# Kernel tuning notes

Hardware: AMD Instinct MI355X
Metric: run time of the kernel (lower is better)

The kernel has to match this reference:

```python
import jax, jax.numpy as jnp
import numpy as np

# ViT-Tiny + Performer attention (eval mode: dropout/droppath are no-ops)
B = 64
IMG, PATCH, GRID = 224, 16, 14
NPATCH, NTOK = 196, 197
EMBED, HEADS, HEAD_DIM = 192, 3, 64
DEPTH, FEAT, MLP, NCLS = 12, 256, 768, 1000
EXIT_IDXS = [4, 8, 12]
LN_EPS = 1e-5


def _ln(x, w, b):
    mu = x.mean(-1, keepdims=True)
    var = ((x - mu) ** 2).mean(-1, keepdims=True)
    return (x - mu) / jnp.sqrt(var + LN_EPS) * w + b


def setup_inputs() -> dict:
    key = jax.random.key(0)
    ks = jax.random.split(key, 16)
    n = lambda k, shape, s=0.02: jax.random.normal(k, shape, jnp.float32) * s
    inp = {}
    inp["x"] = jax.random.normal(ks[0], (B, 3, IMG, IMG), jnp.float32)
    inp["patch_w"] = n(ks[1], (EMBED, 3, PATCH, PATCH))
    inp["patch_b"] = jnp.zeros((EMBED,), jnp.float32)
    inp["pe_norm_w"] = jnp.ones((EMBED,), jnp.float32)
    inp["pe_norm_b"] = jnp.zeros((EMBED,), jnp.float32)
    inp["cls_token"] = n(ks[2], (1, 1, EMBED))
    inp["pos_embed"] = n(ks[3], (1, NTOK, EMBED))
    inp["norm1_w"] = jnp.ones((DEPTH, EMBED), jnp.float32)
    inp["norm1_b"] = jnp.zeros((DEPTH, EMBED), jnp.float32)
    inp["qkv_w"] = n(ks[4], (DEPTH, EMBED, 3 * EMBED))
    inp["qkv_b"] = jnp.zeros((DEPTH, 3 * EMBED), jnp.float32)
    # Gaussian random projection matrix (stands in for the orthogonal RF matrix)
    inp["proj_mat"] = jax.random.normal(ks[5], (DEPTH, FEAT, HEAD_DIM), jnp.float32)
    inp["attn_proj_w"] = n(ks[6], (DEPTH, EMBED, EMBED))
    inp["attn_proj_b"] = jnp.zeros((DEPTH, EMBED), jnp.float32)
    inp["norm2_w"] = jnp.ones((DEPTH, EMBED), jnp.float32)
    inp["norm2_b"] = jnp.zeros((DEPTH, EMBED), jnp.float32)
    inp["fc1_w"] = n(ks[7], (DEPTH, EMBED, MLP))
    inp["fc1_b"] = jnp.zeros((DEPTH, MLP), jnp.float32)
    inp["fc2_w"] = n(ks[8], (DEPTH, MLP, EMBED))
    inp["fc2_b"] = jnp.zeros((DEPTH, EMBED), jnp.float32)
    inp["exit_w"] = n(ks[9], (len(EXIT_IDXS), EMBED, NCLS))
    inp["exit_b"] = jnp.zeros((len(EXIT_IDXS), NCLS), jnp.float32)
    inp["final_norm_w"] = jnp.ones((EMBED,), jnp.float32)
    inp["final_norm_b"] = jnp.zeros((EMBED,), jnp.float32)
    inp["head_w"] = n(ks[10], (EMBED, NCLS))
    inp["head_b"] = jnp.zeros((NCLS,), jnp.float32)
    return inp


def _performer_attn(x, qw, qb, pm, pw, pb):
    Bn, N, C = x.shape
    qkv = (x @ qw + qb).reshape(Bn, N, 3, HEADS, HEAD_DIM).transpose(2, 0, 3, 1, 4)
    q, k, v = qkv[0], qkv[1], qkv[2]  # [B,H,N,d]

    def fmap(t):
        proj = jnp.einsum('bhnd,fd->bhnf', t, pm)  # random-feature projection
        norm_t = jnp.sum(t * t, axis=-1, keepdims=True) / 2.0
        return jnp.exp(proj - norm_t) * (HEAD_DIM ** -0.25)

    pq = fmap(q)  # [B,H,N,F]
    pk = fmap(k)
    k_cumsum = pk.sum(axis=2)  # [B,H,F]
    D_inv = 1.0 / jnp.einsum('bhnf,bhf->bhn', pq, k_cumsum)
    attn = jnp.einsum('bhnf,bhmf->bhnm', pq, pk)  # as in original (materializes NxN)
    out = jnp.einsum('bhnm,bhmd->bhnd', attn, v)
    out = out * D_inv[..., None]
    out = out.transpose(0, 2, 1, 3).reshape(Bn, N, C)
    return out @ pw + pb


def reference(x, patch_w, patch_b, pe_norm_w, pe_norm_b, cls_token, pos_embed,
              norm1_w, norm1_b, qkv_w, qkv_b, proj_mat, attn_proj_w, attn_proj_b,
              norm2_w, norm2_b, fc1_w, fc1_b, fc2_w, fc2_b,
              exit_w, exit_b, final_norm_w, final_norm_b, head_w, head_b):
    Bn = x.shape[0]
    # PatchEmbed: non-overlapping 16x16 conv == reshape + matmul (c,ph,pw order)
    p = x.reshape(Bn, 3, GRID, PATCH, GRID, PATCH).transpose(0, 2, 4, 1, 3, 5)
    p = p.reshape(Bn, NPATCH, 3 * PATCH * PATCH)
    tok = p @ patch_w.reshape(EMBED, -1).T + patch_b
    tok = _ln(tok, pe_norm_w, pe_norm_b)
    cls = jnp.broadcast_to(cls_token, (Bn, 1, EMBED))
    h = jnp.concatenate([cls, tok], axis=1) + pos_embed  # [B,197,192]

    exits = []
    for i in range(DEPTH):
        a = _performer_attn(_ln(h, norm1_w[i], norm1_b[i]), qkv_w[i], qkv_b[i],
                            proj_mat[i], attn_proj_w[i], attn_proj_b[i])
        h = h + a
        m = _ln(h, norm2_w[i], norm2_b[i])
        m = jax.nn.gelu(m @ fc1_w[i] + fc1_b[i], approximate=False) @ fc2_w[i] + fc2_b[i]
        h = h + m
        if (i + 1) in EXIT_IDXS:
            e = EXIT_IDXS.index(i + 1)
            z = h.mean(axis=1)  # AdaptiveAvgPool1d(1) over tokens
            exits.append(z @ exit_w[e] + exit_b[e])

    hf = _ln(h, final_norm_w, final_norm_b)
    logits = hf[:, 0] @ head_w + head_b  # cls-token head
    return (logits, exits[0], exits[1], exits[2])
```

## Files before the change

### kernel.cpp

```cpp
#include <hip/hip_runtime.h>
#include <math.h>

typedef unsigned short u16;
typedef unsigned int u32;
typedef __attribute__((ext_vector_type(8))) short short8;
typedef __attribute__((ext_vector_type(4))) float floatx4;

#define BB 64
#define NTOK 197
#define NPATCH 196
#define EMB 192
#define NH 3
#define HD 64
#define FEAT 256
#define MLPD 768
#define NCLS 1000
#define MTOT (BB*NTOK)
#define MPAT (BB*NPATCH)
#define BHT (BB*NH)

__device__ __forceinline__ u16 f2bf(float x) {
    u32 u = __builtin_bit_cast(u32, x);
    u32 r = u + 0x7FFFu + ((u >> 16) & 1u);
    return (u16)(r >> 16);
}
__device__ __forceinline__ float bf2f(u16 u) {
    return __builtin_bit_cast(float, (u32)u << 16);
}
__device__ __forceinline__ float sqr8bf(uint4 v) {
    float s = 0.f;
    float t;
    t = bf2f((u16)(v.x & 0xffff)); s += t*t;  t = bf2f((u16)(v.x >> 16)); s += t*t;
    t = bf2f((u16)(v.y & 0xffff)); s += t*t;  t = bf2f((u16)(v.y >> 16)); s += t*t;
    t = bf2f((u16)(v.z & 0xffff)); s += t*t;  t = bf2f((u16)(v.z >> 16)); s += t*t;
    t = bf2f((u16)(v.w & 0xffff)); s += t*t;  t = bf2f((u16)(v.w >> 16)); s += t*t;
    return s;
}

__global__ void cvt_bf16(const float* __restrict__ in, u16* __restrict__ out, int n)
{
    const int i = blockIdx.x * 256 + threadIdx.x;
    if (i < n) out[i] = f2bf(in[i]);
}

__global__ void tr_bf16_t(const float* __restrict__ in, u16* __restrict__ out,
                          int R, int C)
{
    __shared__ u16 t[32][33];
    const int l = blockIdx.z;
    const int c0 = blockIdx.x * 32, r0 = blockIdx.y * 32;
    const int tx = threadIdx.x & 31, ty = threadIdx.x >> 5;
    const float* ip = in + ((size_t)l * R + r0) * C + c0;
#pragma unroll
    for (int j = 0; j < 4; ++j)
        t[ty + j*8][tx] = f2bf(ip[(size_t)(ty + j*8) * C + tx]);
    __syncthreads();
    u16* op = out + ((size_t)l * C + c0) * R + r0;
#pragma unroll
    for (int j = 0; j < 4; ++j)
        op[(size_t)(ty + j*8) * R + tx] = t[tx][ty + j*8];
}

__global__ void tr_bf16_g(const float* __restrict__ in, u16* __restrict__ out,
                          int R, int C)
{
    __shared__ u16 t[32][33];
    const int l = blockIdx.z;
    const int c0 = blockIdx.x * 32, r0 = blockIdx.y * 32;
    const int tx = threadIdx.x & 31, ty = threadIdx.x >> 5;
    const float* ip = in + (size_t)l * R * C;
#pragma unroll
    for (int j = 0; j < 4; ++j) {
        const int r = r0 + ty + j*8, c = c0 + tx;
        t[ty + j*8][tx] = (r < R && c < C) ? f2bf(ip[(size_t)r * C + c]) : (u16)0;
    }
    __syncthreads();
    u16* op = out + (size_t)l * C * R;
#pragma unroll
    for (int j = 0; j < 4; ++j) {
        const int c = c0 + ty + j*8, r = r0 + tx;
        if (c < C && r < R)
            op[(size_t)c * R + r] = t[tx][ty + j*8];
    }
}

__global__ __launch_bounds__(256) void gemm_bf16(
    const u16* __restrict__ A, const u16* __restrict__ Bt,
    const float* __restrict__ bias,
    float* __restrict__ Cf, u16* __restrict__ Cb,
    int M, int N, int K, int mode, int ntx)
{
    __shared__ u16 As[128][72];
    __shared__ u16 Bs[64][72];
    const int tid = threadIdx.x;
    const int lane = tid & 63, wave = tid >> 6;
    const int l16 = lane & 15, quad = lane >> 4;
    const int nwg = gridDim.x;
    const int q = nwg >> 3, r = nwg & 7;
    const int xcd = blockIdx.x & 7, jj = blockIdx.x >> 3;
    const int wg = (xcd < r ? xcd * (q + 1) : r * (q + 1) + (xcd - r) * q) + jj;
    const int m0 = (wg / ntx) * 128, n0 = (wg % ntx) * 64;
    const int arow = tid >> 1, aof = (tid & 1) * 32;
    const int brow = tid >> 2, bof = (tid & 3) * 16;

    floatx4 acc[2][4];
#pragma unroll
    for (int i = 0; i < 2; ++i)
#pragma unroll
        for (int j = 0; j < 4; ++j) acc[i][j] = (floatx4){0.f,0.f,0.f,0.f};

    const int gmA = m0 + arow;
    const bool aok = (gmA < M);
    const u16* ap = A + (size_t)gmA * K + aof;
    const u16* bp = Bt + (size_t)(n0 + brow) * K + bof;

    for (int k0 = 0; k0 < K; k0 += 64) {
        uint4 a0 = {0,0,0,0}, a1 = {0,0,0,0}, a2 = {0,0,0,0}, a3 = {0,0,0,0};
        if (aok) {
            a0 = *(const uint4*)(ap + k0);
            a1 = *(const uint4*)(ap + k0 + 8);
            a2 = *(const uint4*)(ap + k0 + 16);
            a3 = *(const uint4*)(ap + k0 + 24);
        }
        const uint4 b0 = *(const uint4*)(bp + k0);
        const uint4 b1 = *(const uint4*)(bp + k0 + 8);
        if (k0) __syncthreads();
        *(uint4*)&As[arow][aof]      = a0;
        *(uint4*)&As[arow][aof + 8]  = a1;
        *(uint4*)&As[arow][aof + 16] = a2;
        *(uint4*)&As[arow][aof + 24] = a3;
        *(uint4*)&Bs[brow][bof]      = b0;
        *(uint4*)&Bs[brow][bof + 8]  = b1;
        __syncthreads();
#pragma unroll
        for (int ks = 0; ks < 2; ++ks) {
            short8 af[2], bf[4];
#pragma unroll
            for (int rf = 0; rf < 2; ++rf)
                af[rf] = *(const short8*)&As[wave*32 + rf*16 + l16][ks*32 + quad*8];
#pragma unroll
            for (int cf = 0; cf < 4; ++cf)
                bf[cf] = *(const short8*)&Bs[cf*16 + l16][ks*32 + quad*8];
#pragma unroll
            for (int rf = 0; rf < 2; ++rf)
#pragma unroll
                for (int cf = 0; cf < 4; ++cf)
                    acc[rf][cf] = __builtin_amdgcn_mfma_f32_16x16x32_bf16(af[rf], bf[cf], acc[rf][cf], 0, 0, 0);
        }
    }

    if (mode == 0) {
        const int rbase = m0 + wave * 32 + quad * 4;
        const int cbase = n0 + l16;
#pragma unroll
        for (int rf = 0; rf < 2; ++rf) {
#pragma unroll
            for (int reg = 0; reg < 4; ++reg) {
                const int gm = rbase + rf * 16 + reg;
                if (gm >= M) continue;
#pragma unroll
                for (int cf = 0; cf < 4; ++cf) {
                    const int gn = cbase + cf * 16;
                    Cf[(size_t)gm * N + gn] = acc[rf][cf][reg] + bias[gn];
                }
            }
        }
        return;
    }

    __syncthreads();
#pragma unroll
    for (int rf = 0; rf < 2; ++rf) {
#pragma unroll
        for (int cf = 0; cf < 4; ++cf) {
            const int lc = cf * 16 + l16;
            const float bia = bias[n0 + lc];
#pragma unroll
            for (int reg = 0; reg < 4; ++reg) {
                const int lr = wave * 32 + rf * 16 + quad * 4 + reg;
                const float v = acc[rf][cf][reg] + bia;
                const int phys = (((lc >> 3) ^ (lr & 7)) << 3) | (lc & 7);
                As[lr][phys] = f2bf(v);
            }
        }
    }
    __syncthreads();
#pragma unroll
    for (int it = 0; it < 4; ++it) {
        const int idx = it * 256 + tid;
        const int row = idx >> 3, c8 = idx & 7;
        const int pc8 = c8 ^ (row & 7);
        const uint4 val = *(const uint4*)&As[row][pc8 * 8];
        const int gm = m0 + row;
        if (gm < M)
            *(uint4*)&Cb[(size_t)gm * N + n0 + c8 * 8] = val;
    }
}

__global__ __launch_bounds__(256) void gemm_ln(
    const u16* __restrict__ A, const u16* __restrict__ Bt,
    const float* __restrict__ bias,
    const float* __restrict__ lnw, const float* __restrict__ lnb,
    float* __restrict__ H, u16* __restrict__ outb, int K)
{
    __shared__ u16 As[32][72];
    __shared__ u16 Bs[192][72];
    __shared__ float red_s[2][32][2];
    const int tid = threadIdx.x;
    const int lane = tid & 63, wave = tid >> 6;
    const int wr = wave & 1;
    const int wc = wave >> 1;
    const int l16 = lane & 15, quad = lane >> 4;
    const int m0 = blockIdx.x * 32;
    const int srowA = tid >> 3, skofA = (tid & 7) * 8;
    const int srow = tid >> 2, skof = (tid & 3) * 16;

    floatx4 acc[6];
#pragma unroll
    for (int j = 0; j < 6; ++j) acc[j] = (floatx4){0.f,0.f,0.f,0.f};

    const u16* ap = A + (size_t)(m0 + srowA) * K + skofA;
    const u16* bp = Bt + (size_t)srow * K + skof;
    const size_t bstep = (size_t)64 * K;

    for (int k0 = 0; k0 < K; k0 += 64) {
        const uint4 a0 = *(const uint4*)(ap + k0);
        const uint4 b0 = *(const uint4*)(bp + k0);
        const uint4 b1 = *(const uint4*)(bp + k0 + 8);
        const uint4 b2 = *(const uint4*)(bp + bstep + k0);
        const uint4 b3 = *(const uint4*)(bp + bstep + k0 + 8);
        const uint4 b4 = *(const uint4*)(bp + 2*bstep + k0);
        const uint4 b5 = *(const uint4*)(bp + 2*bstep + k0 + 8);
        if (k0) __syncthreads();
        *(uint4*)&As[srowA][skofA]         = a0;
        *(uint4*)&Bs[srow][skof]           = b0;
        *(uint4*)&Bs[srow][skof + 8]       = b1;
        *(uint4*)&Bs[srow + 64][skof]      = b2;
        *(uint4*)&Bs[srow + 64][skof + 8]  = b3;
        *(uint4*)&Bs[srow + 128][skof]     = b4;
        *(uint4*)&Bs[srow + 128][skof + 8] = b5;
        __syncthreads();
#pragma unroll
        for (int ks = 0; ks < 2; ++ks) {
            const short8 af = *(const short8*)&As[wr*16 + l16][ks*32 + quad*8];
            short8 bf[6];
#pragma unroll
            for (int cf = 0; cf < 6; ++cf)
                bf[cf] = *(const short8*)&Bs[wc*96 + cf*16 + l16][ks*32 + quad*8];
#pragma unroll
            for (int cf = 0; cf < 6; ++cf)
                acc[cf] = __builtin_amdgcn_mfma_f32_16x16x32_bf16(af, bf[cf], acc[cf], 0, 0, 0);
        }
    }

    float s_[4], q_[4];
#pragma unroll
    for (int reg = 0; reg < 4; ++reg) { s_[reg] = 0.f; q_[reg] = 0.f; }

#pragma unroll
    for (int cf = 0; cf < 6; ++cf) {
        const int gn = wc * 96 + cf * 16 + l16;
        const float bia = bias[gn];
#pragma unroll
        for (int reg = 0; reg < 4; ++reg) {
            const int gm = m0 + wr * 16 + quad * 4 + reg;
            float v = acc[cf][reg] + bia + H[(size_t)gm * EMB + gn];
            H[(size_t)gm * EMB + gn] = v;
            acc[cf][reg] = v;
            s_[reg] += v;
            q_[reg] += v * v;
        }
    }

    if (lnw) {
#pragma unroll
        for (int reg = 0; reg < 4; ++reg) {
            float s = s_[reg], q = q_[reg];
            s += __shfl_xor(s, 1); q += __shfl_xor(q, 1);
            s += __shfl_xor(s, 2); q += __shfl_xor(q, 2);
            s += __shfl_xor(s, 4); q += __shfl_xor(q, 4);
            s += __shfl_xor(s, 8); q += __shfl_xor(q, 8);
            if (l16 == 0) {
                const int rl = wr * 16 + quad * 4 + reg;
                red_s[wc][rl][0] = s;
                red_s[wc][rl][1] = q;
            }
        }
        __syncthreads();
#pragma unroll
        for (int reg = 0; reg < 4; ++reg) {
            const int rl = wr * 16 + quad * 4 + reg;
            const float ts = red_s[0][rl][0] + red_s[1][rl][0];
            const float tq = red_s[0][rl][1] + red_s[1][rl][1];
            const float mu = ts * (1.f / 192.f);
            const float var = tq * (1.f / 192.f) - mu * mu;
            const float rstd = rsqrtf(fmaxf(var, 0.f) + 1e-5f);
            const int gm = m0 + rl;
#pragma unroll
            for (int cf = 0; cf < 6; ++cf) {
                const int gn = wc * 96 + cf * 16 + l16;
                const float y = (acc[cf][reg] - mu) * rstd * lnw[gn] + lnb[gn];
                outb[(size_t)gm * EMB + gn] = f2bf(y);
            }
        }
    }
}

__global__ __launch_bounds__(256) void mlp_ln(
    const u16* __restrict__ A, const u16* __restrict__ W1t,
    const float* __restrict__ b1,
    const u16* __restrict__ W2t, const float* __restrict__ b2,
    const float* __restrict__ lnw, const float* __restrict__ lnb,
    float* __restrict__ H, u16* __restrict__ outb)
{
    __shared__ u16 As[32][200];
    __shared__ u16 W1s[64][200];
    __shared__ u16 W2s[192][72];
    __shared__ u16 Ms[32][72];
    __shared__ float red_s[4][32][2];
    const int tid = threadIdx.x;
    const int lane = tid & 63, wave = tid >> 6;
    const int l16 = lane & 15, quad = lane >> 4;
    const int m0 = blockIdx.x * 32;

    {
        const int row = tid >> 3, cb = (tid & 7) * 24;
        const u16* ap = A + (size_t)(m0 + row) * EMB + cb;
#pragma unroll
        for (int j = 0; j < 3; ++j)
            *(uint4*)&As[row][cb + j * 8] = *(const uint4*)(ap + j * 8);
    }
    __syncthreads();
    short8 af[2][6];
#pragma unroll
    for (int rf = 0; rf < 2; ++rf)
#pragma unroll
        for (int ks = 0; ks < 6; ++ks)
            af[rf][ks] = *(const short8*)&As[rf*16 + l16][ks*32 + quad*8];

    floatx4 acc[2][3];
#pragma unroll
    for (int i = 0; i < 2; ++i)
#pragma unroll
        for (int j = 0; j < 3; ++j) acc[i][j] = (floatx4){0.f,0.f,0.f,0.f};

    for (int c = 0; c < 12; ++c) {
        if (c) __syncthreads();
        {
            const int row = tid >> 2, cb = (tid & 3) * 48;
            const u16* wp = W1t + (size_t)(c * 64 + row) * EMB + cb;
#pragma unroll
            for (int j = 0; j < 6; ++j)
                *(uint4*)&W1s[row][cb + j * 8] = *(const uint4*)(wp + j * 8);
        }
#pragma unroll
        for (int j = 0; j < 6; ++j) {
            const int idx = j * 256 + tid;
            const int e = idx >> 3, o = (idx & 7) * 8;
            *(uint4*)&W2s[e][o] = *(const uint4*)(W2t + (size_t)e * MLPD + c * 64 + o);
        }
        __syncthreads();

        floatx4 mf[2] = {(floatx4){0.f,0.f,0.f,0.f}, (floatx4){0.f,0.f,0.f,0.f}};
#pragma unroll
        for (int ks = 0; ks < 6; ++ks) {
            const short8 w1f = *(const short8*)&W1s[wave*16 + l16][ks*32 + quad*8];
            mf[0] = __builtin_amdgcn_mfma_f32_16x16x32_bf16(af[0][ks], w1f, mf[0], 0, 0, 0);
            mf[1] = __builtin_amdgcn_mfma_f32_16x16x32_bf16(af[1][ks], w1f, mf[1], 0, 0, 0);
        }
        const float bia = b1[c * 64 + wave * 16 + l16];
#pragma unroll
        for (int rf = 0; rf < 2; ++rf)
#pragma unroll
            for (int reg = 0; reg < 4; ++reg) {
                float v = mf[rf][reg] + bia;
                v = 0.5f * v * (1.f + erff(v * 0.70710678118654752f));
                Ms[rf*16 + quad*4 + reg][wave*16 + l16] = f2bf(v);
            }
        __syncthreads();

#pragma unroll
        for (int ks2 = 0; ks2 < 2; ++ks2) {
            short8 a2[2], w2f[3];
#pragma unroll
            for (int rf = 0; rf < 2; ++rf)
                a2[rf] = *(const short8*)&Ms[rf*16 + l16][ks2*32 + quad*8];
#pragma unroll
            for (int cf = 0; cf < 3; ++cf)
                w2f[cf] = *(const short8*)&W2s[wave*48 + cf*16 + l16][ks2*32 + quad*8];
#pragma unroll
            for (int rf = 0; rf < 2; ++rf)
#pragma unroll
                for (int cf = 0; cf < 3; ++cf)
                    acc[rf][cf] = __builtin_amdgcn_mfma_f32_16x16x32_bf16(a2[rf], w2f[cf], acc[rf][cf], 0, 0, 0);
        }
    }

    float s_[2][4], q_[2][4];
#pragma unroll
    for (int rf = 0; rf < 2; ++rf)
#pragma unroll
        for (int reg = 0; reg < 4; ++reg) { s_[rf][reg] = 0.f; q_[rf][reg] = 0.f; }

#pragma unroll
    for (int rf = 0; rf < 2; ++rf) {
#pragma unroll
        for (int cf = 0; cf < 3; ++cf) {
            const int gn = wave * 48 + cf * 16 + l16;
            const float bia = b2[gn];
#pragma unroll
            for (int reg = 0; reg < 4; ++reg) {
                const int gm = m0 + rf * 16 + quad * 4 + reg;
                float v = acc[rf][cf][reg] + bia + H[(size_t)gm * EMB + gn];
                H[(size_t)gm * EMB + gn] = v;
                acc[rf][cf][reg] = v;
                s_[rf][reg] += v;
                q_[rf][reg] += v * v;
            }
        }
    }

    if (lnw) {
#pragma unroll
        for (int rf = 0; rf < 2; ++rf)
#pragma unroll
            for (int reg = 0; reg < 4; ++reg) {
                float s = s_[rf][reg], q = q_[rf][reg];
                s += __shfl_xor(s, 1); q += __shfl_xor(q, 1);
                s += __shfl_xor(s, 2); q += __shfl_xor(q, 2);
                s += __shfl_xor(s, 4); q += __shfl_xor(q, 4);
                s += __shfl_xor(s, 8); q += __shfl_xor(q, 8);
                if (l16 == 0) {
                    const int rl = rf * 16 + quad * 4 + reg;
                    red_s[wave][rl][0] = s;
                    red_s[wave][rl][1] = q;
                }
            }
        __syncthreads();
#pragma unroll
        for (int rf = 0; rf < 2; ++rf) {
#pragma unroll
            for (int reg = 0; reg < 4; ++reg) {
                const int rl = rf * 16 + quad * 4 + reg;
                const float ts = red_s[0][rl][0] + red_s[1][rl][0]
                               + red_s[2][rl][0] + red_s[3][rl][0];
                const float tq = red_s[0][rl][1] + red_s[1][rl][1]
                               + red_s[2][rl][1] + red_s[3][rl][1];
                const float mu = ts * (1.f / 192.f);
                const float var = tq * (1.f / 192.f) - mu * mu;
                const float rstd = rsqrtf(fmaxf(var, 0.f) + 1e-5f);
                const int gm = m0 + rl;
#pragma unroll
                for (int cf = 0; cf < 3; ++cf) {
                    const int gn = wave * 48 + cf * 16 + l16;
                    const float y = (acc[rf][cf][reg] - mu) * rstd * lnw[gn] + lnb[gn];
                    outb[(size_t)gm * EMB + gn] = f2bf(y);
                }
            }
        }
    }
}

__global__ __launch_bounds__(256) void attn_pkv(
    const u16* __restrict__ qkv, const u16* __restrict__ pmb,
    u16* __restrict__ kvT, float* __restrict__ ksum)
{
    __shared__ u16 pm_s[64][72];
    __shared__ u16 kt_s[64][72];
    __shared__ u16 vT_s[64][72];
    __shared__ u16 pkT_s[64][72];
    __shared__ float nrm_s[64];
    __shared__ float ksum_s[64];

    const int tid = threadIdx.x;
    const int lane = tid & 63, wave = tid >> 6;
    const int l16 = lane & 15, quad = lane >> 4;
    const int fq = blockIdx.x, bh = blockIdx.y, b = bh / NH, h = bh % NH;
    const int fwave = wave * 16;
    const int srow = tid >> 2, skof = (tid & 3) * 16;
    const float scale = 0.35355339059327373f;

#pragma unroll
    for (int j = 0; j < 2; ++j) {
        const int flat = j * 256 + tid;
        const int row = flat >> 3, o = (flat & 7) * 8;
        *(uint4*)&pm_s[row][o] = *(const uint4*)(pmb + (size_t)(fq * 64 + row) * 64 + o);
    }
    if (tid < 64) ksum_s[tid] = 0.f;

    floatx4 kv[4];
#pragma unroll
    for (int i = 0; i < 4; ++i) kv[i] = (floatx4){0.f,0.f,0.f,0.f};

    uint4 k0v = {0,0,0,0}, k1v = {0,0,0,0}, v0v = {0,0,0,0}, v1v = {0,0,0,0};
    {
        const u16* kp = qkv + ((size_t)(b * NTOK + srow)) * 576 + 192 + h * 64 + skof;
        k0v = *(const uint4*)kp; k1v = *(const uint4*)(kp + 8);
        v0v = *(const uint4*)(kp + 192); v1v = *(const uint4*)(kp + 200);
    }

    for (int t = 0; t < 4; ++t) {
        const int ncur = t * 64 + srow;
        if (t) __syncthreads();
        *(uint4*)&kt_s[srow][skof]     = k0v;
        *(uint4*)&kt_s[srow][skof + 8] = k1v;
        {
            u16 vv[16];
            vv[0]=(u16)(v0v.x&0xffff);  vv[1]=(u16)(v0v.x>>16);
            vv[2]=(u16)(v0v.y&0xffff);  vv[3]=(u16)(v0v.y>>16);
            vv[4]=(u16)(v0v.z&0xffff);  vv[5]=(u16)(v0v.z>>16);
            vv[6]=(u16)(v0v.w&0xffff);  vv[7]=(u16)(v0v.w>>16);
            vv[8]=(u16)(v1v.x&0xffff);  vv[9]=(u16)(v1v.x>>16);
            vv[10]=(u16)(v1v.y&0xffff); vv[11]=(u16)(v1v.y>>16);
            vv[12]=(u16)(v1v.z&0xffff); vv[13]=(u16)(v1v.z>>16);
            vv[14]=(u16)(v1v.w&0xffff); vv[15]=(u16)(v1v.w>>16);
#pragma unroll
            for (int j = 0; j < 16; ++j) vT_s[skof + j][srow] = vv[j];
        }
        float sq = sqr8bf(k0v) + sqr8bf(k1v);
        sq += __shfl_xor(sq, 1);
        sq += __shfl_xor(sq, 2);
        if ((tid & 3) == 0) nrm_s[srow] = (ncur < NTOK) ? 0.5f * sq : 1e30f;
        __syncthreads();

        if (t < 3) {
            const int n = (t + 1) * 64 + srow;
            k0v = (uint4){0,0,0,0}; k1v = (uint4){0,0,0,0};
            v0v = (uint4){0,0,0,0}; v1v = (uint4){0,0,0,0};
            if (n < NTOK) {
                const u16* kp = qkv + ((size_t)(b * NTOK + n)) * 576 + 192 + h * 64 + skof;
                k0v = *(const uint4*)kp; k1v = *(const uint4*)(kp + 8);
                v0v = *(const uint4*)(kp + 192); v1v = *(const uint4*)(kp + 200);
            }
        }

        floatx4 pa[4];
#pragma unroll
        for (int i = 0; i < 4; ++i) pa[i] = (floatx4){0.f,0.f,0.f,0.f};
#pragma unroll
        for (int ks = 0; ks < 2; ++ks) {
            const short8 bpm = *(const short8*)&pm_s[fwave + l16][ks*32 + quad*8];
#pragma unroll
            for (int rf = 0; rf < 4; ++rf) {
                const short8 a = *(const short8*)&kt_s[rf*16 + l16][ks*32 + quad*8];
                pa[rf] = __builtin_amdgcn_mfma_f32_16x16x32_bf16(a, bpm, pa[rf], 0, 0, 0);
            }
        }

        float ksp = 0.f;
        const int floc = fwave + l16;
#pragma unroll
        for (int rf = 0; rf < 4; ++rf) {
            const int nl = rf * 16 + quad * 4;
            const u16 b0 = f2bf(__expf(pa[rf][0] - nrm_s[nl + 0]) * scale);
            const u16 b1 = f2bf(__expf(pa[rf][1] - nrm_s[nl + 1]) * scale);
            const u16 b2 = f2bf(__expf(pa[rf][2] - nrm_s[nl + 2]) * scale);
            const u16 b3 = f2bf(__expf(pa[rf][3] - nrm_s[nl + 3]) * scale);
            ksp += bf2f(b0) + bf2f(b1) + bf2f(b2) + bf2f(b3);
            *(u32*)&pkT_s[floc][nl]     = (u32)b0 | ((u32)b1 << 16);
            *(u32*)&pkT_s[floc][nl + 2] = (u32)b2 | ((u32)b3 << 16);
        }
        {
            float v = ksp;
            v += __shfl_xor(v, 16);
            v += __shfl_xor(v, 32);
            if (quad == 0) ksum_s[floc] += v;
        }

#pragma unroll
        for (int ks = 0; ks < 2; ++ks) {
            const short8 bpk = *(const short8*)&pkT_s[fwave + l16][ks*32 + quad*8];
#pragma unroll
            for (int rf = 0; rf < 4; ++rf) {
                const short8 a = *(const short8*)&vT_s[rf*16 + l16][ks*32 + quad*8];
                kv[rf] = __builtin_amdgcn_mfma_f32_16x16x32_bf16(a, bpk, kv[rf], 0, 0, 0);
            }
        }
    }

    __syncthreads();
    if (tid < 64) ksum[(size_t)bh * 256 + fq * 64 + tid] = ksum_s[tid];
    const int fg = fq * 64 + fwave + l16;
#pragma unroll
    for (int rf = 0; rf < 4; ++rf) {
#pragma unroll
        for (int reg = 0; reg < 4; ++reg) {
            const int d = rf * 16 + quad * 4 + reg;
            kvT[((size_t)bh * 64 + d) * 256 + fg] = f2bf(kv[rf][reg]);
        }
    }
}

__global__ __launch_bounds__(256) void attn_out(
    const u16* __restrict__ qkv, const u16* __restrict__ pmb,
    const u16* __restrict__ kvT, const float* __restrict__ ksum,
    u16* __restrict__ attn_o)
{
    __shared__ u16 pm_s[256][72];
    __shared__ u16 q_s[64][72];
    __shared__ u16 pq_s[64][264];
    __shared__ u16 kv_s[64][264];
    __shared__ float nrm_s[64];
    __shared__ float den_s[4][64];

    const int tid = threadIdx.x;
    const int lane = tid & 63, wave = tid >> 6;
    const int l16 = lane & 15, quad = lane >> 4;
    const int bh = blockIdx.y, b = bh / NH, h = bh % NH;
    const int n0 = blockIdx.x * 64;
    const int fbase = wave * 64;
    const int srow = tid >> 2, skof = (tid & 3) * 16;
    const float scale = 0.35355339059327373f;

#pragma unroll
    for (int j = 0; j < 8; ++j) {
        const int flat = j * 256 + tid;
        const int f = flat >> 3, o = (flat & 7) * 8;
        *(uint4*)&pm_s[f][o] = *(const uint4*)(pmb + f * 64 + o);
    }
#pragma unroll
    for (int j = 0; j < 8; ++j) {
        const int flat = j * 256 + tid;
        const int d = flat >> 5, o = (flat & 31) * 8;
        *(uint4*)&kv_s[d][o] = *(const uint4*)(kvT + ((size_t)bh * 64 + d) * 256 + o);
    }
    {
        const int n = n0 + srow;
        uint4 q0 = {0,0,0,0}, q1 = {0,0,0,0};
        if (n < NTOK) {
            const u16* qp = qkv + ((size_t)(b * NTOK + n)) * 576 + h * 64 + skof;
            q0 = *(const uint4*)qp; q1 = *(const uint4*)(qp + 8);
        }
        *(uint4*)&q_s[srow][skof]     = q0;
        *(uint4*)&q_s[srow][skof + 8] = q1;
        float sq = sqr8bf(q0) + sqr8bf(q1);
        sq += __shfl_xor(sq, 1);
        sq += __shfl_xor(sq, 2);
        if ((tid & 3) == 0) nrm_s[srow] = (n < NTOK) ? 0.5f * sq : 1e30f;
    }
    float ksr[4];
#pragma unroll
    for (int cf = 0; cf < 4; ++cf)
        ksr[cf] = ksum[(size_t)bh * 256 + fbase + cf * 16 + l16];
    __syncthreads();

    floatx4 pa[4][4];
#pragma unroll
    for (int i = 0; i < 4; ++i)
#pragma unroll
        for (int j = 0; j < 4; ++j) pa[i][j] = (floatx4){0.f,0.f,0.f,0.f};
#pragma unroll
    for (int ks = 0; ks < 2; ++ks) {
        short8 a[4], bb[4];
#pragma unroll
        for (int rf = 0; rf < 4; ++rf)
            a[rf] = *(const short8*)&q_s[rf*16 + l16][ks*32 + quad*8];
#pragma unroll
        for (int cf = 0; cf < 4; ++cf)
            bb[cf] = *(const short8*)&pm_s[fbase + cf*16 + l16][ks*32 + quad*8];
#pragma unroll
        for (int rf = 0; rf < 4; ++rf)
#pragma unroll
            for (int cf = 0; cf < 4; ++cf)
                pa[rf][cf] = __builtin_amdgcn_mfma_f32_16x16x32_bf16(a[rf], bb[cf], pa[rf][cf], 0, 0, 0);
    }

    float dpart[16];
#pragma unroll
    for (int i = 0; i < 16; ++i) dpart[i] = 0.f;
#pragma unroll
    for (int rf = 0; rf < 4; ++rf) {
        const int nl = rf * 16 + quad * 4;
        const float nr0 = nrm_s[nl + 0], nr1 = nrm_s[nl + 1];
        const float nr2 = nrm_s[nl + 2], nr3 = nrm_s[nl + 3];
#pragma unroll
        for (int cf = 0; cf < 4; ++cf) {
            const int f = fbase + cf * 16 + l16;
            const u16 b0 = f2bf(__expf(pa[rf][cf][0] - nr0) * scale);
            const u16 b1 = f2bf(__expf(pa[rf][cf][1] - nr1) * scale);
            const u16 b2 = f2bf(__expf(pa[rf][cf][2] - nr2) * scale);
            const u16 b3 = f2bf(__expf(pa[rf][cf][3] - nr3) * scale);
            pq_s[nl + 0][f] = b0;
            pq_s[nl + 1][f] = b1;
            pq_s[nl + 2][f] = b2;
            pq_s[nl + 3][f] = b3;
            dpart[rf*4 + 0] += bf2f(b0) * ksr[cf];
            dpart[rf*4 + 1] += bf2f(b1) * ksr[cf];
            dpart[rf*4 + 2] += bf2f(b2) * ksr[cf];
            dpart[rf*4 + 3] += bf2f(b3) * ksr[cf];
        }
    }
#pragma unroll
    for (int i = 0; i < 16; ++i) {
        float d = dpart[i];
        d += __shfl_xor(d, 1); d += __shfl_xor(d, 2);
        d += __shfl_xor(d, 4); d += __shfl_xor(d, 8);
        dpart[i] = d;
    }
    if (l16 == 0) {
#pragma unroll
        for (int rf = 0; rf < 4; ++rf)
#pragma unroll
            for (int reg = 0; reg < 4; ++reg)
                den_s[wave][rf*16 + quad*4 + reg] = dpart[rf*4 + reg];
    }
    __syncthreads();

    const int wr = wave & 1, wc = wave >> 1;
    floatx4 oc[2][2];
#pragma unroll
    for (int i = 0; i < 2; ++i)
#pragma unroll
        for (int j = 0; j < 2; ++j) oc[i][j] = (floatx4){0.f,0.f,0.f,0.f};
#pragma unroll
    for (int ks = 0; ks < 8; ++ks) {
        short8 a[2], bb[2];
#pragma unroll
        for (int rf = 0; rf < 2; ++rf)
            a[rf] = *(const short8*)&pq_s[wr*32 + rf*16 + l16][ks*32 + quad*8];
#pragma unroll
        for (int cf = 0; cf < 2; ++cf)
            bb[cf] = *(const short8*)&kv_s[wc*32 + cf*16 + l16][ks*32 + quad*8];
#pragma unroll
        for (int rf = 0; rf < 2; ++rf)
#pragma unroll
            for (int cf = 0; cf < 2; ++cf)
                oc[rf][cf] = __builtin_amdgcn_mfma_f32_16x16x32_bf16(a[rf], bb[cf], oc[rf][cf], 0, 0, 0);
    }

#pragma unroll
    for (int rf = 0; rf < 2; ++rf) {
#pragma unroll
        for (int reg = 0; reg < 4; ++reg) {
            const int nl = wr*32 + rf*16 + quad*4 + reg;
            const int gn = n0 + nl;
            if (gn >= NTOK) continue;
            const float di = 1.f / (den_s[0][nl] + den_s[1][nl] + den_s[2][nl] + den_s[3][nl]);
#pragma unroll
            for (int cf = 0; cf < 2; ++cf) {
                const int d = wc*32 + cf*16 + l16;
                attn_o[((size_t)(b * NTOK + gn)) * EMB + h * 64 + d] =
                    f2bf(oc[rf][cf][reg] * di);
            }
        }
    }
}

__global__ void im2col_kernel(const float* __restrict__ x, u16* __restrict__ p, int total)
{
    const int i = blockIdx.x * 256 + threadIdx.x;
    if (i >= total) return;
    const int col = i % 768, row = i / 768;
    const int px = col & 15, py = (col >> 4) & 15, c = col >> 8;
    const int gx = row % 14, gy = (row / 14) % 14, b = row / 196;
    p[i] = f2bf(x[((size_t)(b * 3 + c) * 224 + gy * 16 + py) * 224 + gx * 16 + px]);
}

__global__ void embed_finish(const float* __restrict__ tok, const float* __restrict__ cls,
                             const float* __restrict__ pos, const float* __restrict__ w,
                             const float* __restrict__ b,
                             const float* __restrict__ n1w, const float* __restrict__ n1b,
                             float* __restrict__ h, u16* __restrict__ outb)
{
    const int wid = threadIdx.x >> 6, lane = threadIdx.x & 63;
    const int r = blockIdx.x * 4 + wid;
    if (r >= MTOT) return;
    const int bb = r / NTOK, t = r % NTOK;
    float y0, y1, y2;
    if (t == 0) {
        y0 = cls[lane]       + pos[lane];
        y1 = cls[lane + 64]  + pos[lane + 64];
        y2 = cls[lane + 128] + pos[lane + 128];
    } else {
        const float* p = tok + ((size_t)bb * NPATCH + (t - 1)) * EMB;
        float x0 = p[lane], x1 = p[lane + 64], x2 = p[lane + 128];
        float s = x0 + x1 + x2;
#pragma unroll
        for (int off = 32; off; off >>= 1) s += __shfl_xor(s, off);
        const float mu = s * (1.f / 192.f);
        const float d0 = x0 - mu, d1 = x1 - mu, d2 = x2 - mu;
        float v = d0 * d0 + d1 * d1 + d2 * d2;
#pragma unroll
        for (int off = 32; off; off >>= 1) v += __shfl_xor(v, off);
        const float rstd = rsqrtf(v * (1.f / 192.f) + 1e-5f);
        const float* pr = pos + (size_t)t * EMB;
        y0 = d0 * rstd * w[lane]       + b[lane]       + pr[lane];
        y1 = d1 * rstd * w[lane + 64]  + b[lane + 64]  + pr[lane + 64];
        y2 = d2 * rstd * w[lane + 128] + b[lane + 128] + pr[lane + 128];
    }
    float* q = h + (size_t)r * EMB;
    q[lane] = y0; q[lane + 64] = y1; q[lane + 128] = y2;
    float s2 = y0 + y1 + y2;
#pragma unroll
    for (int off = 32; off; off >>= 1) s2 += __shfl_xor(s2, off);
    const float mu2 = s2 * (1.f / 192.f);
    const float e0 = y0 - mu2, e1 = y1 - mu2, e2 = y2 - mu2;
    float v2 = e0 * e0 + e1 * e1 + e2 * e2;
#pragma unroll
    for (int off = 32; off; off >>= 1) v2 += __shfl_xor(v2, off);
    const float rstd2 = rsqrtf(v2 * (1.f / 192.f) + 1e-5f);
    u16* o = outb + (size_t)r * EMB;
    o[lane]       = f2bf(e0 * rstd2 * n1w[lane]       + n1b[lane]);
    o[lane + 64]  = f2bf(e1 * rstd2 * n1w[lane + 64]  + n1b[lane + 64]);
    o[lane + 128] = f2bf(e2 * rstd2 * n1w[lane + 128] + n1b[lane + 128]);
}

__global__ void ln192(const float* __restrict__ in, int in_stride,
                      const float* __restrict__ w, const float* __restrict__ b,
                      u16* __restrict__ outb, float* __restrict__ outf, int rows)
{
    const int wid = threadIdx.x >> 6, lane = threadIdx.x & 63;
    const int r = blockIdx.x * 4 + wid;
    if (r >= rows) return;
    const float* p = in + (size_t)r * in_stride;
    float x0 = p[lane], x1 = p[lane + 64], x2 = p[lane + 128];
    float s = x0 + x1 + x2;
#pragma unroll
    for (int off = 32; off; off >>= 1) s += __shfl_xor(s, off);
    const float mu = s * (1.f / 192.f);
    const float d0 = x0 - mu, d1 = x1 - mu, d2 = x2 - mu;
    float v = d0 * d0 + d1 * d1 + d2 * d2;
#pragma unroll
    for (int off = 32; off; off >>= 1) v += __shfl_xor(v, off);
    const float rstd = rsqrtf(v * (1.f / 192.f) + 1e-5f);
    const float y0 = d0 * rstd * w[lane]       + b[lane];
    const float y1 = d1 * rstd * w[lane + 64]  + b[lane + 64];
    const float y2 = d2 * rstd * w[lane + 128] + b[lane + 128];
    if (outf) {
        float* q = outf + (size_t)r * EMB;
        q[lane] = y0; q[lane + 64] = y1; q[lane + 128] = y2;
    } else {
        u16* q = outb + (size_t)r * EMB;
        q[lane] = f2bf(y0); q[lane + 64] = f2bf(y1); q[lane + 128] = f2bf(y2);
    }
}

__global__ __launch_bounds__(256) void gemm_cls(
    const u16* __restrict__ A, const u16* __restrict__ Bt,
    const float* __restrict__ bias, float* __restrict__ C,
    int N, int K)
{
    __shared__ u16 As[64][72];
    __shared__ u16 Bs[64][72];
    const int tid = threadIdx.x;
    const int lane = tid & 63, wave = tid >> 6;
    const int wr = wave & 1, wc = wave >> 1;
    const int l16 = lane & 15, quad = lane >> 4;
    const int n0 = blockIdx.x * 64;
    const int srow = tid >> 2, skof = (tid & 3) * 16;

    floatx4 acc[2][2];
#pragma unroll
    for (int i = 0; i < 2; ++i)
#pragma unroll
        for (int j = 0; j < 2; ++j) acc[i][j] = (floatx4){0.f,0.f,0.f,0.f};

    const u16* ap = A + (size_t)srow * K + skof;
    int brow_g = n0 + srow;  if (brow_g > N - 1) brow_g = N - 1;
    const u16* bp = Bt + (size_t)brow_g * K + skof;

    for (int k0 = 0; k0 < K; k0 += 64) {
        const uint4 a0 = *(const uint4*)(ap + k0);
        const uint4 a1 = *(const uint4*)(ap + k0 + 8);
        const uint4 b0 = *(const uint4*)(bp + k0);
        const uint4 b1 = *(const uint4*)(bp + k0 + 8);
        if (k0) __syncthreads();
        *(uint4*)&As[srow][skof]     = a0;
        *(uint4*)&As[srow][skof + 8] = a1;
        *(uint4*)&Bs[srow][skof]     = b0;
        *(uint4*)&Bs[srow][skof + 8] = b1;
        __syncthreads();
#pragma unroll
        for (int ks = 0; ks < 2; ++ks) {
            short8 af[2], bf[2];
#pragma unroll
            for (int rf = 0; rf < 2; ++rf)
                af[rf] = *(const short8*)&As[wr*32 + rf*16 + l16][ks*32 + quad*8];
#pragma unroll
            for (int cf = 0; cf < 2; ++cf)
                bf[cf] = *(const short8*)&Bs[wc*32 + cf*16 + l16][ks*32 + quad*8];
#pragma unroll
            for (int rf = 0; rf < 2; ++rf)
#pragma unroll
                for (int cf = 0; cf < 2; ++cf)
                    acc[rf][cf] = __builtin_amdgcn_mfma_f32_16x16x32_bf16(af[rf], bf[cf], acc[rf][cf], 0, 0, 0);
        }
    }

#pragma unroll
    for (int rf = 0; rf < 2; ++rf) {
#pragma unroll
        for (int reg = 0; reg < 4; ++reg) {
            const int gm = wr*32 + rf*16 + quad*4 + reg;
#pragma unroll
            for (int cf = 0; cf < 2; ++cf) {
                const int gn = n0 + wc*32 + cf*16 + l16;
                if (gn < N)
                    C[(size_t)gm * N + gn] = acc[rf][cf][reg] + bias[gn];
            }
        }
    }
}

__global__ void pool_kernel(const float* __restrict__ h, u16* __restrict__ pooled)
{
    __shared__ float red[192];
    const int b = blockIdx.x;
    const int slice = threadIdx.x / 192;
    const int e = threadIdx.x % 192;
    float s = 0.f;
    for (int n = slice; n < NTOK; n += 2)
        s += h[((size_t)(b * NTOK + n)) * EMB + e];
    if (slice == 1) red[e] = s;
    __syncthreads();
    if (slice == 0)
        pooled[b * EMB + e] = f2bf((s + red[e]) * (1.f / 197.f));
}

extern "C" void kernel_launch(void* const* d_in, const int* in_sizes, int n_in,
                              void* d_out, int out_size, void* d_ws, size_t ws_size,
                              hipStream_t stream)
{
    const float* x          = (const float*)d_in[0];
    const float* patch_w    = (const float*)d_in[1];
    const float* patch_b    = (const float*)d_in[2];
    const float* pe_norm_w  = (const float*)d_in[3];
    const float* pe_norm_b  = (const float*)d_in[4];
    const float* cls_token  = (const float*)d_in[5];
    const float* pos_embed  = (const float*)d_in[6];
    const float* norm1_w    = (const float*)d_in[7];
    const float* norm1_b    = (const float*)d_in[8];
    const float* qkv_w      = (const float*)d_in[9];
    const float* qkv_b      = (const float*)d_in[10];
    const float* proj_mat   = (const float*)d_in[11];
    const float* attn_pw    = (const float*)d_in[12];
    const float* attn_pb    = (const float*)d_in[13];
    const float* norm2_w    = (const float*)d_in[14];
    const float* norm2_b    = (const float*)d_in[15];
    const float* fc1_w      = (const float*)d_in[16];
    const float* fc1_b      = (const float*)d_in[17];
    const float* fc2_w      = (const float*)d_in[18];
    const float* fc2_b      = (const float*)d_in[19];
    const float* exit_w     = (const float*)d_in[20];
    const float* exit_b     = (const float*)d_in[21];
    const float* fnorm_w    = (const float*)d_in[22];
    const float* fnorm_b    = (const float*)d_in[23];
    const float* head_w     = (const float*)d_in[24];
    const float* head_b     = (const float*)d_in[25];
    float* out = (float*)d_out;

    float* ws = (float*)d_ws;
    float* H     = ws + 0;
    u16*   QKVB  = (u16*)(ws + 2420736);
    u16*   XLNB  = (u16*)(ws + 6051840);
    u16*   EXWT  = (u16*)(ws + 7262208);
    u16*   HWT   = (u16*)(ws + 7550208);
    u16*   POOLB = (u16*)(ws + 7646208);
    u16*   KVT   = (u16*)(ws + 19968000);
    u16*   MIDB  = (u16*)(ws + 21540864);
    u16*   ATNB  = (u16*)(ws + 26382336);
    float* KSUM  = ws + 27617280;
    u16*   QKVWT = (u16*)(ws + 27666432);
    u16*   APWT  = (u16*)(ws + 28329984);
    u16*   F1WT  = (u16*)(ws + 28551168);
    u16*   F2WT  = (u16*)(ws + 29435904);
    u16*   PATWB = (u16*)(ws + 30320640);
    u16*   PMB   = (u16*)(ws + 30394368);
    u16*   P_IMB = MIDB;
    float* TOK   = (float*)QKVB;

    if (ws_size < (size_t)30492672 * sizeof(float)) return;

    cvt_bf16<<<(147456 + 255) / 256, 256, 0, stream>>>(patch_w, PATWB, 147456);
    cvt_bf16<<<(196608 + 255) / 256, 256, 0, stream>>>(proj_mat, PMB, 196608);
    tr_bf16_t<<<dim3(18, 6, 12), 256, 0, stream>>>(qkv_w,   QKVWT, 192, 576);
    tr_bf16_t<<<dim3(6, 6, 12),  256, 0, stream>>>(attn_pw, APWT,  192, 192);
    tr_bf16_t<<<dim3(24, 6, 12), 256, 0, stream>>>(fc1_w,   F1WT,  192, 768);
    tr_bf16_t<<<dim3(6, 24, 12), 256, 0, stream>>>(fc2_w,   F2WT,  768, 192);
    tr_bf16_g<<<dim3(32, 6, 3), 256, 0, stream>>>(exit_w, EXWT, 192, 1000);
    tr_bf16_g<<<dim3(32, 6, 1), 256, 0, stream>>>(head_w, HWT,  192, 1000);

    im2col_kernel<<<(MPAT * 768 + 255) / 256, 256, 0, stream>>>(x, P_IMB, MPAT * 768);
    gemm_bf16<<<294, 256, 0, stream>>>(P_IMB, PATWB, patch_b,
                                       TOK, nullptr, MPAT, EMB, 768, 0, 3);
    embed_finish<<<(MTOT + 3) / 4, 256, 0, stream>>>(TOK, cls_token, pos_embed,
                                                     pe_norm_w, pe_norm_b,
                                                     norm1_w, norm1_b, H, XLNB);

    for (int i = 0; i < 12; ++i) {
        const u16* qwt  = QKVWT + (size_t)i * 576 * 192;
        const u16* pwt  = APWT  + (size_t)i * 192 * 192;
        const u16* f1wt = F1WT  + (size_t)i * 768 * 192;
        const u16* f2wt = F2WT  + (size_t)i * 192 * 768;
        const u16* pmb  = PMB   + (size_t)i * 256 * 64;
        const float* qb  = qkv_b   + (size_t)i * 576;
        const float* pb  = attn_pb + (size_t)i * 192;
        const float* f1b = fc1_b   + (size_t)i * 768;

        gemm_bf16<<<891, 256, 0, stream>>>(XLNB, qwt, qb,
                                           nullptr, QKVB, MTOT, 576, 192, 3, 9);
        attn_pkv<<<dim3(4, BHT), 256, 0, stream>>>(QKVB, pmb, KVT, KSUM);
        attn_out<<<dim3(4, BHT), 256, 0, stream>>>(QKVB, pmb, KVT, KSUM, ATNB);
        gemm_ln<<<394, 256, 0, stream>>>(ATNB, pwt, pb,
                                         norm2_w + (size_t)i * EMB, norm2_b + (size_t)i * EMB,
                                         H, XLNB, EMB);
        const float* nw = (i < 11) ? norm1_w + (size_t)(i + 1) * EMB : nullptr;
        const float* nb = (i < 11) ? norm1_b + (size_t)(i + 1) * EMB : nullptr;
        mlp_ln<<<394, 256, 0, stream>>>(XLNB, f1wt, f1b, f2wt,
                                        fc2_b + (size_t)i * 192, nw, nb, H, XLNB);

        const int e = (i == 3) ? 0 : (i == 7) ? 1 : (i == 11) ? 2 : -1;
        if (e >= 0) {
            pool_kernel<<<BB, 384, 0, stream>>>(H, POOLB);
            gemm_cls<<<16, 256, 0, stream>>>(POOLB, EXWT + (size_t)e * 1000 * 192,
                                             exit_b + (size_t)e * 1000,
                                             out + (size_t)(1 + e) * BB * NCLS,
                                             NCLS, EMB);
        }
    }

    ln192<<<(BB + 3) / 4, 256, 0, stream>>>(H, NTOK * EMB, fnorm_w, fnorm_b,
                                            XLNB, nullptr, BB);
    gemm_cls<<<16, 256, 0, stream>>>(XLNB, HWT, head_b, out, NCLS, EMB);
}
```

Before: 1.350 ms.

## Fuse next layer's QKV projection into the MLP+LayerNorm kernel epilogue

The mlp_ln kernel now keeps the freshly normalized bf16 rows for its 32-row tile in shared memory and immediately multiplies them by the next layer's QKV weights. It writes the 576-wide qkv output directly, so the standalone QKV GEMM launch is needed only for layer 0. This removes 11 kernel launches and the re-read of the normalized activations from global memory. In exchange, each of the 394 blocks now streams the full 576x192 QKV weight matrix through shared memory serially, with extra barriers and only 4 waves per tile, which lengthens the critical path of mlp_ln.

```diff
diff --git a/kernel.cpp b/kernel.cpp
--- a/kernel.cpp
+++ b/kernel.cpp
@@ -311,7 +311,9 @@
     const float* __restrict__ b1,
     const u16* __restrict__ W2t, const float* __restrict__ b2,
     const float* __restrict__ lnw, const float* __restrict__ lnb,
-    float* __restrict__ H, u16* __restrict__ outb)
+    float* __restrict__ H, u16* __restrict__ outb,
+    const u16* __restrict__ qwt, const float* __restrict__ qb,
+    u16* __restrict__ qkv_out)
 {
     __shared__ u16 As[32][200];
     __shared__ u16 W1s[64][200];
@@ -454,8 +456,45 @@
                 for (int cf = 0; cf < 3; ++cf) {
                     const int gn = wave * 48 + cf * 16 + l16;
                     const float y = (acc[rf][cf][reg] - mu) * rstd * lnw[gn] + lnb[gn];
-                    outb[(size_t)gm * EMB + gn] = f2bf(y);
+                    const u16 yb = f2bf(y);
+                    outb[(size_t)gm * EMB + gn] = yb;
+                    if (qkv_out) As[rl][gn] = yb;
                 }
+            }
+        }
+    }
+
+    if (lnw && qkv_out) {
+        __syncthreads();
+        for (int c = 0; c < 9; ++c) {
+            {
+                const int row = tid >> 2, cb = (tid & 3) * 48;
+                const u16* wp = qwt + (size_t)(c * 64 + row) * EMB + cb;
+#pragma unroll
+                for (int j = 0; j < 6; ++j)
+                    *(uint4*)&W1s[row][cb + j * 8] = *(const uint4*)(wp + j * 8);
+            }
+            __syncthreads();
+            floatx4 acc2[2] = {(floatx4){0.f,0.f,0.f,0.f}, (floatx4){0.f,0.f,0.f,0.f}};
+#pragma unroll
+            for (int ks = 0; ks < 6; ++ks) {
+                const short8 wf = *(const short8*)&W1s[wave*16 + l16][ks*32 + quad*8];
+                const short8 a0 = *(const short8*)&As[l16][ks*32 + quad*8];
+                const short8 a1 = *(const short8*)&As[16 + l16][ks*32 + quad*8];
+                acc2[0] = __builtin_amdgcn_mfma_f32_16x16x32_bf16(a0, wf, acc2[0], 0, 0, 0);
+                acc2[1] = __builtin_amdgcn_mfma_f32_16x16x32_bf16(a1, wf, acc2[1], 0, 0, 0);
+            }
+            const float bia = qb[c * 64 + wave * 16 + l16];
+#pragma unroll
+            for (int rf = 0; rf < 2; ++rf)
+#pragma unroll
+                for (int reg = 0; reg < 4; ++reg)
+                    Ms[rf*16 + quad*4 + reg][wave*16 + l16] = f2bf(acc2[rf][reg] + bia);
+            __syncthreads();
+            {
+                const int row = tid >> 3, c8 = tid & 7;
+                const uint4 val = *(const uint4*)&Ms[row][c8 * 8];
+                *(uint4*)&qkv_out[(size_t)(m0 + row) * 576 + c * 64 + c8 * 8] = val;
             }
         }
     }
@@ -988,17 +1027,17 @@
                                                      norm1_w, norm1_b, H, XLNB);
 
     for (int i = 0; i < 12; ++i) {
-        const u16* qwt  = QKVWT + (size_t)i * 576 * 192;
         const u16* pwt  = APWT  + (size_t)i * 192 * 192;
         const u16* f1wt = F1WT  + (size_t)i * 768 * 192;
         const u16* f2wt = F2WT  + (size_t)i * 192 * 768;
         const u16* pmb  = PMB   + (size_t)i * 256 * 64;
-        const float* qb  = qkv_b   + (size_t)i * 576;
         const float* pb  = attn_pb + (size_t)i * 192;
         const float* f1b = fc1_b   + (size_t)i * 768;
 
-        gemm_bf16<<<891, 256, 0, stream>>>(XLNB, qwt, qb,
-                                           nullptr, QKVB, MTOT, 576, 192, 3, 9);
+        if (i == 0) {
+            gemm_bf16<<<891, 256, 0, stream>>>(XLNB, QKVWT, qkv_b,
+                                               nullptr, QKVB, MTOT, 576, 192, 3, 9);
+        }
         attn_pkv<<<dim3(4, BHT), 256, 0, stream>>>(QKVB, pmb, KVT, KSUM);
         attn_out<<<dim3(4, BHT), 256, 0, stream>>>(QKVB, pmb, KVT, KSUM, ATNB);
         gemm_ln<<<394, 256, 0, stream>>>(ATNB, pwt, pb,
@@ -1006,8 +1045,11 @@
                                          H, XLNB, EMB);
         const float* nw = (i < 11) ? norm1_w + (size_t)(i + 1) * EMB : nullptr;
         const float* nb = (i < 11) ? norm1_b + (size_t)(i + 1) * EMB : nullptr;
+        const u16* qwt_n  = (i < 11) ? QKVWT + (size_t)(i + 1) * 576 * 192 : nullptr;
+        const float* qb_n = (i < 11) ? qkv_b + (size_t)(i + 1) * 576 : nullptr;
         mlp_ln<<<394, 256, 0, stream>>>(XLNB, f1wt, f1b, f2wt,
-                                        fc2_b + (size_t)i * 192, nw, nb, H, XLNB);
+                                        fc2_b + (size_t)i * 192, nw, nb, H, XLNB,
+                                        qwt_n, qb_n, (i < 11) ? QKVB : nullptr);
 
         const int e = (i == 3) ? 0 : (i == 7) ? 1 : (i == 11) ? 2 : -1;
         if (e >= 0) {
```

Result: no change. 1.367 ms (+1.2%).
